# Kernel tuning notes

Measured on AMD Instinct MI355X. Metric: run time of the kernel, lower is better.

## Reference

```python
import math
import jax, jax.numpy as jnp
import numpy as np

N, S, E, H = 8, 1024, 768, 12  # batch, seq_len, n_embed, n_head


def setup_inputs() -> dict:
    key = jax.random.key(0)
    ks = jax.random.split(key, 10)
    s = 1.0 / math.sqrt(E)
    x = jax.random.normal(ks[0], (N, S, E), dtype=jnp.float32)
    # per-head full-width projections, stacked over heads: [H, E, E] (Linear weight layout [out, in])
    Wq = jax.random.normal(ks[1], (H, E, E), dtype=jnp.float32) * s
    Wk = jax.random.normal(ks[2], (H, E, E), dtype=jnp.float32) * s
    Wv = jax.random.normal(ks[3], (H, E, E), dtype=jnp.float32) * s
    bq = jax.random.normal(ks[4], (H, E), dtype=jnp.float32) * s
    bk = jax.random.normal(ks[5], (H, E), dtype=jnp.float32) * s
    bv = jax.random.normal(ks[6], (H, E), dtype=jnp.float32) * s
    Wc = jax.random.normal(ks[7], (E, H * E), dtype=jnp.float32) * (1.0 / math.sqrt(H * E))
    bc = jax.random.normal(ks[8], (E,), dtype=jnp.float32) * s
    return {"x": x, "Wq": Wq, "bq": bq, "Wk": Wk, "bk": bk, "Wv": Wv, "bv": bv, "Wc": Wc, "bc": bc}


def reference(x, Wq, bq, Wk, bk, Wv, bv, Wc, bc):
    # Full-width QKV per head: [H, N, S, E]
    q = jnp.einsum('nse,hde->hnsd', x, Wq) + bq[:, None, None, :]
    k = jnp.einsum('nse,hde->hnsd', x, Wk) + bk[:, None, None, :]
    v = jnp.einsum('nse,hde->hnsd', x, Wv) + bv[:, None, None, :]
    # scores scaled by sqrt(n_embed) (source quirk: full n_embed, not head_dim)
    scores = jnp.einsum('hnsd,hntd->hnst', q, k) / math.sqrt(E)
    causal = jnp.tril(jnp.ones((S, S), dtype=bool))
    scores = jnp.where(causal[None, None, :, :], scores, -jnp.inf)
    # dropout applied before softmax in source; p=0 (eval) -> identity
    attn = jax.nn.softmax(scores, axis=-1)
    heads = jnp.einsum('hnst,hntd->hnsd', attn, v)  # [H, N, S, E]
    concat = jnp.transpose(heads, (1, 2, 0, 3)).reshape(N, S, H * E)
    return concat @ Wc.T + bc
```

## Files before the change

kernel.cpp:

```cpp
#include <hip/hip_runtime.h>
#include <hip/hip_bf16.h>
#include <stdint.h>

#define SEQ    1024
#define NBAT   8
#define EMB    768
#define NHEAD  12
#define MROWS  (NBAT*SEQ)
#define SCALE_S 0.03608439182435161f

typedef unsigned short u16;
typedef __attribute__((ext_vector_type(8))) short bf16x8;
typedef __attribute__((ext_vector_type(4))) float f32x4;

typedef void __attribute__((address_space(1)))* gas_ptr;
typedef void __attribute__((address_space(3)))* las_ptr;

__device__ __forceinline__ void gload16(const void* g, void* l) {
  __builtin_amdgcn_global_load_lds((gas_ptr)(void*)g, (las_ptr)l, 16, 0, 0);
}

#define VMCNT0 asm volatile("s_waitcnt vmcnt(0)" ::: "memory")
#define VMCNT2 asm volatile("s_waitcnt vmcnt(2)" ::: "memory")
#define VMCNT4 asm volatile("s_waitcnt vmcnt(4)" ::: "memory")
#define LGKM0  asm volatile("s_waitcnt lgkmcnt(0)" ::: "memory")
#define BARRIER asm volatile("s_barrier" ::: "memory")

__device__ __forceinline__ u16 f2bf(float f) {
  union { float f; uint32_t u; } a; a.f = f;
  uint32_t r = a.u + 0x7fffu + ((a.u >> 16) & 1u);
  return (u16)(r >> 16);
}
__device__ __forceinline__ uint32_t pack2(float a, float b) {
  return (uint32_t)f2bf(a) | ((uint32_t)f2bf(b) << 16);
}

__global__ void k_cvt(const float* __restrict__ s, u16* __restrict__ d, long n) {
  long i = ((long)blockIdx.x*blockDim.x + threadIdx.x)*8;
  if (i >= n) return;
  float4 a = *(const float4*)(s+i);
  float4 b = *(const float4*)(s+i+4);
  uint4 o; o.x = pack2(a.x,a.y); o.y = pack2(a.z,a.w);
  o.z = pack2(b.x,b.y); o.w = pack2(b.z,b.w);
  *(uint4*)(d+i) = o;
}

__global__ void k_cvt3(const float* __restrict__ s0, const float* __restrict__ s1,
                       const float* __restrict__ s2, u16* __restrict__ d0,
                       u16* __restrict__ d1, u16* __restrict__ d2, long n) {
  const float* s = blockIdx.z == 0 ? s0 : (blockIdx.z == 1 ? s1 : s2);
  u16* d = blockIdx.z == 0 ? d0 : (blockIdx.z == 1 ? d1 : d2);
  long i = ((long)blockIdx.x*blockDim.x + threadIdx.x)*8;
  if (i >= n) return;
  float4 a = *(const float4*)(s+i);
  float4 b = *(const float4*)(s+i+4);
  uint4 o; o.x = pack2(a.x,a.y); o.y = pack2(a.z,a.w);
  o.z = pack2(b.x,b.y); o.w = pack2(b.z,b.w);
  *(uint4*)(d+i) = o;
}

__global__ void k_cvtwc(const float* __restrict__ wc, u16* __restrict__ d, int Gi, int h0) {
  long ncol = (long)Gi*EMB;
  long i = ((long)blockIdx.x*blockDim.x + threadIdx.x)*4;
  if (i >= 768*ncol) return;
  long eo = i / ncol, c = i - eo*ncol;
  long g = c / EMB, dd = c - g*EMB;
  const float* s = wc + eo*(long)(NHEAD*EMB) + (h0+g)*EMB + dd;
  float4 a = *(const float4*)s;
  uint2 o; o.x = pack2(a.x,a.y); o.y = pack2(a.z,a.w);
  *(uint2*)(d+i) = o;
}

__global__ __launch_bounds__(256) void k_gemm(
    const u16* __restrict__ A, long a_hs, int lda,
    const u16* __restrict__ B, long b_hs, int ldb, int K,
    u16* Cb, float* Cf, long c_hs, int ldc,
    const float* __restrict__ bias, const float* __restrict__ bias2,
    long bias_hs, int gsplit, int mode, int swapxy)
{
  __shared__ u16 lsA[3*4096];
  __shared__ u16 lsB[3*4096];
  int g = blockIdx.z;
  const u16* Ag = A + (long)g*a_hs;
  const u16* Bg = B + (long)g*b_hs;
  int tm = swapxy ? blockIdx.y : blockIdx.x;
  int tn = swapxy ? blockIdx.x : blockIdx.y;
  int m0 = tm*128, n0 = tn*128;
  int tid = threadIdx.x;
  int w = tid >> 6, l = tid & 63;

  int srow = l >> 2;
  int scol = ((l & 3) ^ ((l >> 3) & 3)) * 8;
  const u16* ga0 = Ag + (long)(m0 + (2*w)*16   + srow)*lda + scol;
  const u16* ga1 = Ag + (long)(m0 + (2*w+1)*16 + srow)*lda + scol;
  const u16* gb0 = Bg + (long)(n0 + (2*w)*16   + srow)*ldb + scol;
  const u16* gb1 = Bg + (long)(n0 + (2*w+1)*16 + srow)*ldb + scol;

#define GSTAGE(k0, buf) do { \
    gload16(ga0 + (k0), lsA + (buf)*4096 + (2*w)*512); \
    gload16(ga1 + (k0), lsA + (buf)*4096 + (2*w+1)*512); \
    gload16(gb0 + (k0), lsB + (buf)*4096 + (2*w)*512); \
    gload16(gb1 + (k0), lsB + (buf)*4096 + (2*w+1)*512); \
  } while(0)

  f32x4 acc[4][4];
  #pragma unroll
  for (int i = 0; i < 4; ++i)
    #pragma unroll
    for (int j = 0; j < 4; ++j) acc[i][j] = (f32x4)0.0f;

  int wr = w >> 1, wc_ = w & 1;
  int frow = l & 15;
  int sp = (l >> 4) ^ ((frow >> 1) & 3);
  int aoff[4], boff[4];
  #pragma unroll
  for (int i = 0; i < 4; ++i) {
    aoff[i] = (wr*64 + i*16 + frow)*32 + sp*8;
    boff[i] = (wc_*64 + i*16 + frow)*32 + sp*8;
  }

  int nt = K >> 5;
  GSTAGE(0, 0);
  GSTAGE(32, 1);
  VMCNT4; BARRIER;
  int cur = 0;
  for (int t = 0; t < nt; ++t) {
    if (t + 2 < nt) {
      int nb = cur + 2; if (nb >= 3) nb -= 3;
      GSTAGE((t+2) << 5, nb);
    }
    const u16* la = lsA + cur*4096;
    const u16* lb = lsB + cur*4096;
    bf16x8 af[4], bfr[4];
    #pragma unroll
    for (int i = 0; i < 4; ++i) af[i] = *(const bf16x8*)(la + aoff[i]);
    #pragma unroll
    for (int j = 0; j < 4; ++j) bfr[j] = *(const bf16x8*)(lb + boff[j]);
    #pragma unroll
    for (int i = 0; i < 4; ++i)
      #pragma unroll
      for (int j = 0; j < 4; ++j)
        acc[i][j] = __builtin_amdgcn_mfma_f32_16x16x32_bf16(af[i], bfr[j], acc[i][j], 0, 0, 0);
    if (t + 2 < nt) { VMCNT4; } else { VMCNT0; }
    LGKM0; BARRIER;
    cur = (cur == 2) ? 0 : cur + 1;
  }
#undef GSTAGE

  u16* Cbg = Cb ? Cb + (long)g*c_hs : (u16*)0;
  const float* bsel = (g < gsplit) ? bias : bias2;
  long gi = (g < gsplit) ? g : g - gsplit;
  const float* bs = bsel ? bsel + gi*bias_hs : (const float*)0;
  int rl = (l >> 4)*4, cl = l & 15;
  #pragma unroll
  for (int i = 0; i < 4; ++i) {
    #pragma unroll
    for (int j = 0; j < 4; ++j) {
      int rb = m0 + wr*64 + i*16 + rl;
      int cb = n0 + wc_*64 + j*16 + cl;
      float cbv = 0.f;
      if ((mode == 0 || mode == 2) && bs) cbv = bs[cb];
      #pragma unroll
      for (int r = 0; r < 4; ++r) {
        int rr = rb + r;
        float v = acc[i][j][r];
        v += (mode == 1) ? bs[rr] : cbv;
        size_t idx = (size_t)rr*(size_t)ldc + cb;
        if (mode <= 1) Cbg[idx] = f2bf(v);
        else if (mode == 2) Cf[idx] = v;
        else Cf[idx] += v;
      }
    }
  }
}

__global__ __launch_bounds__(512, 2) void k_attn(
    const u16* __restrict__ qb, const u16* __restrict__ kb,
    const u16* __restrict__ vtb, u16* __restrict__ hb, int ldh)
{
  __shared__ u16 kls[3*8192];
  __shared__ u16 vls[3*8192];
  __shared__ float s_t[64*68];
  __shared__ u16 p_t[64*64];
  __shared__ float e_s[64];

  int b = blockIdx.x;
  int xcd = b & 7, kk_ = b >> 3;
  int gn = xcd + 8*(kk_ >> 3), pair = kk_ & 7;
  int g = gn >> 3, n = gn & 7;

  const u16* Q  = qb  + (size_t)g*MROWS*EMB + (size_t)n*SEQ*EMB;
  const u16* Kp = kb  + (size_t)g*MROWS*EMB + (size_t)n*SEQ*EMB;
  const u16* Vt = vtb + (size_t)g*EMB*MROWS + (size_t)n*SEQ;
  u16* H = hb + (size_t)(n*SEQ)*ldh + (size_t)g*EMB;

  int tid = threadIdx.x;
  int w = tid >> 6, l = tid & 63;
  int qg = w >> 1;
  int cg = w & 1;
  int frow = l & 15;
  int fsw = frow & 7;
  int srow = tid >> 3;
  int sphys = tid & 7;
  int scol = ((sphys ^ (srow & 7)) << 3);

#define KSTAGE(base, pc, buf) do { \
    gload16((base) + (pc)*128,      kls + (buf)*8192 + w*512); \
    gload16((base) + (pc)*128 + 64, kls + (buf)*8192 + 4096 + w*512); \
  } while(0)
#define VSTAGE(vc, buf) do { \
    gload16(Vs + (size_t)((vc)*128)*MROWS,      vls + (buf)*8192 + w*512); \
    gload16(Vs + (size_t)((vc)*128 + 64)*MROWS, vls + (buf)*8192 + 4096 + w*512); \
  } while(0)

  for (int half = 0; half < 2; ++half) {
    int qt = half ? 15 - pair : pair;
    int q0 = qt * 64;
    int nt = qt + 1;

    f32x4 acc[6][4];
    #pragma unroll
    for (int i = 0; i < 6; ++i)
      #pragma unroll
      for (int j = 0; j < 4; ++j) acc[i][j] = (f32x4)0.0f;
    float m_reg = -1e30f, l_reg = 0.f;

    const u16* Qs = Q + (size_t)(q0 + srow)*EMB + scol;
    bf16x8 qreg[12][2];
    KSTAGE(Qs, 0, 0);
    KSTAGE(Qs, 1, 1);
    VMCNT2; BARRIER;
    #pragma unroll
    for (int pc = 0; pc < 6; ++pc) {
      if (pc < 4) KSTAGE(Qs, pc+2, (pc+2)%3);
      const u16* qb_ = kls + (pc%3)*8192;
      #pragma unroll
      for (int kk2 = 0; kk2 < 2; ++kk2)
        #pragma unroll
        for (int kkl = 0; kkl < 2; ++kkl)
          qreg[2*pc + kk2][kkl] = *(const bf16x8*)(qb_ + kk2*4096 + (qg*16 + frow)*64
                                                   + (((kkl*4 + (l>>4)) ^ fsw) << 3));
      if (pc < 4) { VMCNT2; } else if (pc == 4) { VMCNT0; }
      LGKM0; BARRIER;
    }

    for (int tt = 0; tt < nt; ++tt) {
      int t0 = tt*64;
      const u16* Ks = Kp + (size_t)(t0 + srow)*EMB + scol;
      const u16* Vs = Vt + (size_t)srow*MROWS + t0 + scol;
      if (tt == 0) { KSTAGE(Ks, 0, 0); KSTAGE(Ks, 1, 1); }
      VMCNT2; BARRIER;

      f32x4 sacc[2]; sacc[0] = (f32x4)0.0f; sacc[1] = (f32x4)0.0f;
      #pragma unroll
      for (int c = 0; c < 6; ++c) {
        if (c < 4)       KSTAGE(Ks, c+2, (c+2)%3);
        else if (c == 4) VSTAGE(0, 0);
        else             VSTAGE(1, 1);
        const u16* kb_ = kls + (c%3)*8192;
        __builtin_amdgcn_s_setprio(1);
        #pragma unroll
        for (int kk2 = 0; kk2 < 2; ++kk2) {
          #pragma unroll
          for (int kkl = 0; kkl < 2; ++kkl) {
            int so = ((kkl*4 + (l>>4)) ^ fsw) << 3;
            bf16x8 aq = qreg[2*c + kk2][kkl];
            #pragma unroll
            for (int cc = 0; cc < 2; ++cc) {
              bf16x8 bk_ = *(const bf16x8*)(kb_ + kk2*4096 + ((cg*2 + cc)*16 + frow)*64 + so);
              sacc[cc] = __builtin_amdgcn_mfma_f32_16x16x32_bf16(aq, bk_, sacc[cc], 0, 0, 0);
            }
          }
        }
        __builtin_amdgcn_s_setprio(0);
        if (c < 5) { VMCNT2; LGKM0; BARRIER; }
      }

      #pragma unroll
      for (int cc = 0; cc < 2; ++cc)
        #pragma unroll
        for (int r = 0; r < 4; ++r)
          s_t[(qg*16 + (l>>4)*4 + r)*68 + cg*32 + cc*16 + (l&15)] = sacc[cc][r]*SCALE_S;
      LGKM0; BARRIER;
      {
        int qglob = q0 + srow;
        int cbase = t0 + sphys*8;
        float v[8]; float mx = -1e30f;
        #pragma unroll
        for (int j = 0; j < 8; ++j) {
          float s = s_t[srow*68 + sphys*8 + j];
          if (cbase + j > qglob) s = -1e30f;
          v[j] = s; mx = fmaxf(mx, s);
        }
        mx = fmaxf(mx, __shfl_xor(mx, 1));
        mx = fmaxf(mx, __shfl_xor(mx, 2));
        mx = fmaxf(mx, __shfl_xor(mx, 4));
        float mn = fmaxf(m_reg, mx);
        float esc = __expf(m_reg - mn);
        float ps = 0.f; u16 pk[8];
        #pragma unroll
        for (int j = 0; j < 8; ++j) { float p = __expf(v[j] - mn); ps += p; pk[j] = f2bf(p); }
        ps += __shfl_xor(ps, 1); ps += __shfl_xor(ps, 2); ps += __shfl_xor(ps, 4);
        l_reg = l_reg*esc + ps; m_reg = mn;
        if (sphys == 0) e_s[srow] = esc;
        uint4 pv;
        pv.x = (uint32_t)pk[0] | ((uint32_t)pk[1] << 16);
        pv.y = (uint32_t)pk[2] | ((uint32_t)pk[3] << 16);
        pv.z = (uint32_t)pk[4] | ((uint32_t)pk[5] << 16);
        pv.w = (uint32_t)pk[6] | ((uint32_t)pk[7] << 16);
        *(uint4*)(p_t + srow*64 + ((sphys ^ (srow & 7)) << 3)) = pv;
      }
      VMCNT2; LGKM0; BARRIER;
      float er[4];
      #pragma unroll
      for (int r = 0; r < 4; ++r) er[r] = e_s[qg*16 + (l>>4)*4 + r];
      #pragma unroll
      for (int i = 0; i < 6; ++i)
        #pragma unroll
        for (int j = 0; j < 4; ++j)
          #pragma unroll
          for (int r = 0; r < 4; ++r) acc[i][j][r] *= er[r];
      bf16x8 pa[2];
      #pragma unroll
      for (int kk = 0; kk < 2; ++kk)
        pa[kk] = *(const bf16x8*)(p_t + (qg*16 + frow)*64 + (((kk*4 + (l>>4)) ^ fsw) << 3));
      bool stage_next = (tt + 1 < nt);
      const u16* Ks2 = Kp + (size_t)(t0 + 64 + srow)*EMB + scol;
      #pragma unroll
      for (int c = 0; c < 6; ++c) {
        if (c < 4)            VSTAGE(c+2, (c+2)%3);
        else if (stage_next)  { if (c == 4) KSTAGE(Ks2, 0, 0); else KSTAGE(Ks2, 1, 1); }
        const u16* vb_ = vls + (c%3)*8192;
        __builtin_amdgcn_s_setprio(1);
        #pragma unroll
        for (int cf = 0; cf < 4; ++cf) {
          #pragma unroll
          for (int kk = 0; kk < 2; ++kk) {
            bf16x8 vbf = *(const bf16x8*)(vb_ + (cg*64 + cf*16 + frow)*64 + (((kk*4 + (l>>4)) ^ fsw) << 3));
            acc[c][cf] = __builtin_amdgcn_mfma_f32_16x16x32_bf16(pa[kk], vbf, acc[c][cf], 0, 0, 0);
          }
        }
        __builtin_amdgcn_s_setprio(0);
        if (c < 4)      { VMCNT2; LGKM0; BARRIER; }
        else if (c == 4){ if (stage_next) { VMCNT2; } else { VMCNT0; } LGKM0; BARRIER; }
      }
    }
    if (sphys == 0) e_s[srow] = l_reg;
    LGKM0; BARRIER;
    float linv[4];
    #pragma unroll
    for (int r = 0; r < 4; ++r) linv[r] = 1.0f / e_s[qg*16 + (l>>4)*4 + r];
    #pragma unroll
    for (int i = 0; i < 6; ++i)
      #pragma unroll
      for (int j = 0; j < 4; ++j) {
        int col = i*128 + cg*64 + j*16 + (l & 15);
        #pragma unroll
        for (int r = 0; r < 4; ++r) {
          int row = q0 + qg*16 + (l>>4)*4 + r;
          H[(size_t)row*ldh + col] = f2bf(acc[i][j][r]*linv[r]);
        }
      }
    BARRIER;
  }
#undef KSTAGE
#undef VSTAGE
}

extern "C" void kernel_launch(void* const* d_in, const int* in_sizes, int n_in,
                              void* d_out, int out_size, void* d_ws, size_t ws_size,
                              hipStream_t stream) {
  const float* x  = (const float*)d_in[0];
  const float* Wq = (const float*)d_in[1];
  const float* bq = (const float*)d_in[2];
  const float* Wk = (const float*)d_in[3];
  const float* bk = (const float*)d_in[4];
  const float* Wv = (const float*)d_in[5];
  const float* bv = (const float*)d_in[6];
  const float* Wc = (const float*)d_in[7];
  const float* bc = (const float*)d_in[8];
  float* out = (float*)d_out;

  const size_t XB  = (size_t)MROWS*EMB*sizeof(u16);
  const size_t WHB = (size_t)EMB*EMB*sizeof(u16);
  const size_t per_g = 4*WHB + 4*XB;
  long long avail = (long long)ws_size - (long long)XB - 4096;
  int G = (int)(avail / (long long)per_g);
  if (G < 1) G = 1;
  if (G > NHEAD) G = NHEAD;

  char* ws = (char*)d_ws;
  u16* xb  = (u16*)ws;  ws += XB;
  u16* wqb = (u16*)ws;  ws += (size_t)(2*G)*WHB;
  u16* wvb = (u16*)ws;  ws += (size_t)G*WHB;
  u16* wcb = (u16*)ws;  ws += (size_t)G*WHB;
  u16* qb  = (u16*)ws;  ws += (size_t)(2*G)*XB;
  u16* vtb = (u16*)ws;  ws += (size_t)G*XB;
  u16* hbf = (u16*)ws;  ws += (size_t)G*XB;

  k_cvt<<<dim3(3072), dim3(256), 0, stream>>>(x, xb, (long)MROWS*EMB);

  for (int h0 = 0; h0 < NHEAD; h0 += G) {
    int Gi = (G < NHEAD - h0) ? G : (NHEAD - h0);
    long nw = (long)Gi*EMB*EMB;
    k_cvt3<<<dim3((unsigned)(nw/8/256), 1, 3), dim3(256), 0, stream>>>(
        Wq + (size_t)h0*EMB*EMB, Wk + (size_t)h0*EMB*EMB, Wv + (size_t)h0*EMB*EMB,
        wqb, wqb + (size_t)Gi*EMB*EMB, wvb, nw);
    k_cvtwc<<<dim3((unsigned)((768L*Gi*EMB/4)/256)), dim3(256), 0, stream>>>(Wc, wcb, Gi, h0);
    k_gemm<<<dim3(64, 6, 2*Gi), dim3(256), 0, stream>>>(
        xb, 0L, EMB, wqb, (long)EMB*EMB, EMB, EMB,
        qb, (float*)0, (long)MROWS*EMB, EMB,
        bq + (size_t)h0*EMB, bk + (size_t)h0*EMB, (long)EMB, Gi, 0, 0);
    k_gemm<<<dim3(64, 6, Gi), dim3(256), 0, stream>>>(
        wvb, (long)EMB*EMB, EMB, xb, 0L, EMB, EMB,
        vtb, (float*)0, (long)MROWS*EMB, MROWS,
        bv + (size_t)h0*EMB, (const float*)0, (long)EMB, 9999, 1, 1);
    k_attn<<<dim3(8*NBAT*Gi), dim3(512), 0, stream>>>(
        qb, qb + (size_t)Gi*MROWS*EMB, vtb, hbf, Gi*EMB);
    k_gemm<<<dim3(64, 6, 1), dim3(256), 0, stream>>>(
        hbf, 0L, Gi*EMB, wcb, 0L, Gi*EMB, Gi*EMB,
        (u16*)0, out, 0L, EMB,
        (h0 == 0 ? bc : (const float*)0), (const float*)0, 0L, 9999,
        (h0 == 0 ? 2 : 3), 0);
  }
}
```

Baseline: 1.221 ms.

## Add 256x256-tile bf16 MFMA GEMM for Q/K and V^T projections

Adds a k_gemm256 kernel with 512 threads and 256x256 output tiles, double-buffered through LDS with direct global-to-LDS loads and an XOR swizzle. The Q/K projection and the transposed V projection now use it in place of the 128x128 k_gemm. Larger tiles raise arithmetic intensity and cut redundant loads of A and B. In exchange they need much more LDS (128KB) and many accumulator registers, which may limit occupancy, and the grid has fewer, larger blocks. The epilogue stores are scattered 2-byte writes.

```diff
diff --git a/kernel.cpp b/kernel.cpp
--- a/kernel.cpp
+++ b/kernel.cpp
@@ -69,6 +69,104 @@
   float4 a = *(const float4*)s;
   uint2 o; o.x = pack2(a.x,a.y); o.y = pack2(a.z,a.w);
   *(uint2*)(d+i) = o;
+}
+
+__global__ __launch_bounds__(512, 2) void k_gemm256(
+    const u16* __restrict__ A, int lda,
+    const u16* __restrict__ B, int ldb, int K,
+    u16* __restrict__ Cb, long c_hs, int ldc,
+    const float* __restrict__ bias, const float* __restrict__ bias2,
+    int gsplit, int mode)
+{
+  __shared__ u16 lsA[2*16384];
+  __shared__ u16 lsB[2*16384];
+
+  int m0 = blockIdx.x * 256;
+  int n0 = blockIdx.y * 256;
+  int tid = threadIdx.x;
+  int w = tid >> 6, l = tid & 63;
+  int wr = w >> 2, wc = w & 3;
+
+  const u16* gA = A + (size_t)(m0 + 32*w + (l>>3))*lda + (((l&7) ^ (l>>3)) << 3);
+  const u16* gB = B + (size_t)(n0 + 32*w + (l>>3))*ldb + (((l&7) ^ (l>>3)) << 3);
+
+#define STAGE256(t, buf) do { \
+    int k0_ = (t)*64; \
+    _Pragma("unroll") \
+    for (int c_ = 0; c_ < 4; ++c_) \
+      gload16(gA + (size_t)(c_*8)*lda + k0_, lsA + (buf)*16384 + (32*w + 8*c_)*64); \
+    _Pragma("unroll") \
+    for (int c_ = 0; c_ < 4; ++c_) \
+      gload16(gB + (size_t)(c_*8)*ldb + k0_, lsB + (buf)*16384 + (32*w + 8*c_)*64); \
+  } while(0)
+
+  f32x4 acc[8][4];
+  #pragma unroll
+  for (int i = 0; i < 8; ++i)
+    #pragma unroll
+    for (int j = 0; j < 4; ++j) acc[i][j] = (f32x4)0.0f;
+
+  int nt = K >> 6;
+  STAGE256(0, 0);
+  for (int t = 0; t < nt; ++t) {
+    VMCNT0; BARRIER;
+    if (t + 1 < nt) STAGE256(t+1, (t+1)&1);
+    const u16* la = lsA + (t&1)*16384;
+    const u16* lb = lsB + (t&1)*16384;
+    #pragma unroll
+    for (int ks = 0; ks < 2; ++ks) {
+      int off = (((4*ks + (l>>4)) ^ (l&7)) << 3);
+      bf16x8 af[8], bf_[4];
+      #pragma unroll
+      for (int fi = 0; fi < 8; ++fi)
+        af[fi] = *(const bf16x8*)(la + (wr*128 + fi*16 + (l&15))*64 + off);
+      #pragma unroll
+      for (int fj = 0; fj < 4; ++fj)
+        bf_[fj] = *(const bf16x8*)(lb + (wc*64 + fj*16 + (l&15))*64 + off);
+      __builtin_amdgcn_s_setprio(1);
+      #pragma unroll
+      for (int fi = 0; fi < 8; ++fi)
+        #pragma unroll
+        for (int fj = 0; fj < 4; ++fj)
+          acc[fi][fj] = __builtin_amdgcn_mfma_f32_16x16x32_bf16(af[fi], bf_[fj], acc[fi][fj], 0, 0, 0);
+      __builtin_amdgcn_s_setprio(0);
+    }
+  }
+#undef STAGE256
+
+  if (mode == 0) {
+    int s = n0 / 768;
+    int dbase = n0 - s*768 + wc*64;
+    const float* bsl = (s < gsplit) ? bias + (size_t)s*768 : bias2 + (size_t)(s - gsplit)*768;
+    u16* Cs = Cb + (size_t)s*c_hs;
+    #pragma unroll
+    for (int fj = 0; fj < 4; ++fj) {
+      int dcol = dbase + fj*16 + (l&15);
+      float bb = bsl[dcol];
+      #pragma unroll
+      for (int fi = 0; fi < 8; ++fi) {
+        #pragma unroll
+        for (int r = 0; r < 4; ++r) {
+          int row = m0 + wr*128 + fi*16 + (l>>4)*4 + r;
+          Cs[(size_t)row*768 + dcol] = f2bf(acc[fi][fj][r] + bb);
+        }
+      }
+    }
+  } else {
+    #pragma unroll
+    for (int fi = 0; fi < 8; ++fi) {
+      #pragma unroll
+      for (int r = 0; r < 4; ++r) {
+        int row = m0 + wr*128 + fi*16 + (l>>4)*4 + r;
+        float bb = bias[row];
+        #pragma unroll
+        for (int fj = 0; fj < 4; ++fj) {
+          int cbn = n0 + wc*64 + fj*16 + (l&15);
+          Cb[(size_t)row*ldc + cbn] = f2bf(acc[fi][fj][r] + bb);
+        }
+      }
+    }
+  }
 }
 
 __global__ __launch_bounds__(256) void k_gemm(
@@ -407,14 +505,14 @@
         Wq + (size_t)h0*EMB*EMB, Wk + (size_t)h0*EMB*EMB, Wv + (size_t)h0*EMB*EMB,
         wqb, wqb + (size_t)Gi*EMB*EMB, wvb, nw);
     k_cvtwc<<<dim3((unsigned)((768L*Gi*EMB/4)/256)), dim3(256), 0, stream>>>(Wc, wcb, Gi, h0);
-    k_gemm<<<dim3(64, 6, 2*Gi), dim3(256), 0, stream>>>(
-        xb, 0L, EMB, wqb, (long)EMB*EMB, EMB, EMB,
-        qb, (float*)0, (long)MROWS*EMB, EMB,
-        bq + (size_t)h0*EMB, bk + (size_t)h0*EMB, (long)EMB, Gi, 0, 0);
-    k_gemm<<<dim3(64, 6, Gi), dim3(256), 0, stream>>>(
-        wvb, (long)EMB*EMB, EMB, xb, 0L, EMB, EMB,
-        vtb, (float*)0, (long)MROWS*EMB, MROWS,
-        bv + (size_t)h0*EMB, (const float*)0, (long)EMB, 9999, 1, 1);
+    k_gemm256<<<dim3(32, 6*Gi), dim3(512), 0, stream>>>(
+        xb, EMB, wqb, EMB, EMB,
+        qb, (long)MROWS*EMB, 768,
+        bq + (size_t)h0*EMB, bk + (size_t)h0*EMB, Gi, 0);
+    k_gemm256<<<dim3(3*Gi, 32), dim3(512), 0, stream>>>(
+        wvb, EMB, xb, EMB, EMB,
+        vtb, 0L, MROWS,
+        bv + (size_t)h0*EMB, (const float*)0, 9999, 1);
     k_attn<<<dim3(8*NBAT*Gi), dim3(512), 0, stream>>>(
         qb, qb + (size_t)Gi*MROWS*EMB, vtb, hbf, Gi*EMB);
     k_gemm<<<dim3(64, 6, 1), dim3(256), 0, stream>>>(
```

Result: faster. 1.144 ms (-6.2%).
